# Kernel optimization log

Measured on AMD Instinct MI355X. Metric: run time of the kernel, lower is better.

## Reference

```python
import jax, jax.numpy as jnp
import numpy as np

N, M = 100000, 800000
F_IN, F_E, H = 64, 16, 64
T_NODE, T_EDGE = 2, 3
HEAD_DIM = 16.0


def setup_inputs() -> dict:
    key = jax.random.key(0)
    ks = jax.random.split(key, 16)
    inp = {
        "x": jax.random.normal(ks[0], (N, F_IN), jnp.float32),
        "edge_feat": jax.random.normal(ks[1], (M, F_E), jnp.float32),
        "node_type": jax.random.randint(ks[2], (N,), 0, T_NODE, jnp.int32),
        "edge_src": jax.random.randint(ks[3], (M,), 0, N, jnp.int32),
        "edge_dst": jax.random.randint(ks[4], (M,), 0, N, jnp.int32),
        "edge_type": jax.random.randint(ks[5], (M,), 0, T_EDGE, jnp.int32),
    }
    s_n = 1.0 / np.sqrt(F_IN)
    s_e = 1.0 / np.sqrt(F_E)
    for i, name in enumerate(["W1", "W2", "W3", "W4"]):
        inp[name] = jax.random.normal(ks[6 + i], (T_NODE, F_IN, H), jnp.float32) * s_n
        inp["b" + name[1]] = jax.random.normal(ks[10 + i], (T_NODE, H), jnp.float32) * 0.01
    inp["W5"] = jax.random.normal(ks[14], (T_EDGE, F_E, H), jnp.float32) * s_e
    inp["b5"] = jax.random.normal(ks[15], (T_EDGE, H), jnp.float32) * 0.01
    return inp


def _node_proj(x, W, b, node_type):
    # per-node-type linear: [T,F,H] weights, select row per node type
    p = jnp.einsum('nf,tfh->tnh', x, W) + b[:, None, :]      # [T,N,H]
    return jnp.take_along_axis(p, node_type[None, :, None], axis=0)[0]  # [N,H]


def reference(x, edge_feat, W1, b1, W2, b2, W3, b3, W4, b4, W5, b5,
              node_type, edge_src, edge_dst, edge_type):
    n = x.shape[0]
    h1 = _node_proj(x, W1, b1, node_type)
    h2 = _node_proj(x, W2, b2, node_type)
    h3 = _node_proj(x, W3, b3, node_type)
    h4 = _node_proj(x, W4, b4, node_type)
    # per-edge-type linear via weight gather (F_E is small)
    w5e = jnp.einsum('mf,mfh->mh', edge_feat, W5[edge_type]) + b5[edge_type]  # [M,H]
    # scalar attention logit per edge (w3_i . (w4_j + w5_ij)) / sqrt(head_dim)
    num = jnp.sum(h3[edge_dst] * (h4[edge_src] + w5e), axis=-1)  # [M]
    # softmax over a single scalar per edge == 1.0 exactly (faithful to source)
    score = jax.nn.softmax((num / jnp.sqrt(HEAD_DIM))[:, None], axis=-1)[:, 0]  # [M]
    msg = score[:, None] * (h2[edge_src] + w5e)                  # [M,H]
    out = h1 + jax.ops.segment_sum(msg, edge_dst, num_segments=n)
    return out
```

## Files before the change

### kernel.cpp

```cpp
#include <hip/hip_runtime.h>


#define CAP 16
#define OVF_CAP 32768

typedef __attribute__((ext_vector_type(8))) short short8;
typedef __attribute__((ext_vector_type(4))) float f32x4;

__device__ __forceinline__ float b2f(unsigned short u) {
    union { unsigned v; float f; } x; x.v = ((unsigned)u) << 16; return x.f;
}
__device__ __forceinline__ unsigned short f2b(float f) {
    union { float f; unsigned v; } x; x.f = f;
    unsigned u = x.v;
    unsigned r = (u + 0x7FFFu + ((u >> 16) & 1u)) >> 16;
    return (unsigned short)r;
}

__global__ __launch_bounds__(256) void k1_gemm_scatter(
    const float* __restrict__ x, const int* __restrict__ nt,
    const float* __restrict__ W1, const float* __restrict__ b1,
    const float* __restrict__ W2, const float* __restrict__ b2,
    const int* __restrict__ esrc, const int* __restrict__ edst,
    const int* __restrict__ etype,
    int* __restrict__ cnt32, int* __restrict__ ovfCnt,
    int4* __restrict__ ovf, int2* __restrict__ rec,
    float* __restrict__ out, unsigned short* __restrict__ h2b,
    int N, int M)
{
    __shared__ __align__(16) unsigned short sx[128 * 72];
    __shared__ __align__(16) unsigned short sw[4][64 * 72];
    __shared__ int snt[128];

    int tid = threadIdx.x;

    if (blockIdx.x & 1) {
        int e0 = (blockIdx.x >> 1) * 1024 + tid;
        int dd[4], ssrc[4], tty[4];
        bool v[4];
#pragma unroll
        for (int j = 0; j < 4; ++j) {
            int e = e0 + j * 256;
            v[j] = e < M;
            int ec = v[j] ? e : 0;
            dd[j]   = edst[ec];
            ssrc[j] = esrc[ec];
            tty[j]  = etype[ec];
        }
        int pos[4];
#pragma unroll
        for (int j = 0; j < 4; ++j)
            if (v[j]) pos[j] = atomicAdd(&cnt32[dd[j]], 1);
#pragma unroll
        for (int j = 0; j < 4; ++j) {
            if (!v[j]) continue;
            int packed = ssrc[j] | (tty[j] << 20);
            int e = e0 + j * 256;
            if (pos[j] < CAP) {
                rec[dd[j] * CAP + pos[j]] = make_int2(packed, e);
            } else {
                int slot = atomicAdd(ovfCnt, 1);
                if (slot < OVF_CAP) ovf[slot] = make_int4(packed, e, dd[j], 0);
            }
        }
        return;
    }

    int rowbase = (blockIdx.x >> 1) * 128;

    const float* Wm0 = W1;
    const float* Wm1 = W1 + 4096;
    const float* Wm2 = W2;
    const float* Wm3 = W2 + 4096;
#pragma unroll
    for (int j = 0; j < 4; ++j) {
        int k  = (tid >> 4) + j * 16;
        int n4 = (tid & 15) * 4;
        float4 w0 = *(const float4*)&Wm0[k * 64 + n4];
        float4 w1v = *(const float4*)&Wm1[k * 64 + n4];
        float4 w2v = *(const float4*)&Wm2[k * 64 + n4];
        float4 w3 = *(const float4*)&Wm3[k * 64 + n4];
        sw[0][(n4 + 0) * 72 + k] = f2b(w0.x);
        sw[0][(n4 + 1) * 72 + k] = f2b(w0.y);
        sw[0][(n4 + 2) * 72 + k] = f2b(w0.z);
        sw[0][(n4 + 3) * 72 + k] = f2b(w0.w);
        sw[1][(n4 + 0) * 72 + k] = f2b(w1v.x);
        sw[1][(n4 + 1) * 72 + k] = f2b(w1v.y);
        sw[1][(n4 + 2) * 72 + k] = f2b(w1v.z);
        sw[1][(n4 + 3) * 72 + k] = f2b(w1v.w);
        sw[2][(n4 + 0) * 72 + k] = f2b(w2v.x);
        sw[2][(n4 + 1) * 72 + k] = f2b(w2v.y);
        sw[2][(n4 + 2) * 72 + k] = f2b(w2v.z);
        sw[2][(n4 + 3) * 72 + k] = f2b(w2v.w);
        sw[3][(n4 + 0) * 72 + k] = f2b(w3.x);
        sw[3][(n4 + 1) * 72 + k] = f2b(w3.y);
        sw[3][(n4 + 2) * 72 + k] = f2b(w3.z);
        sw[3][(n4 + 3) * 72 + k] = f2b(w3.w);
    }

    if (tid < 128) {
        int r = rowbase + tid;
        snt[tid] = (r < N) ? nt[r] : 0;
    }

    int fr = (tid & 15) * 4;
    int ir = tid >> 4;
#pragma unroll
    for (int it = 0; it < 8; ++it) {
        int i = it * 16 + ir;
        int r = rowbase + i;
        float4 v = make_float4(0.f, 0.f, 0.f, 0.f);
        if (r < N) v = *(const float4*)&x[(size_t)r * 64 + fr];
        ushort4 p;
        p.x = f2b(v.x); p.y = f2b(v.y); p.z = f2b(v.z); p.w = f2b(v.w);
        *(ushort4*)&sx[i * 72 + fr] = p;
    }
    __syncthreads();

    int lane = tid & 63;
    int wid  = tid >> 6;
    int q    = lane >> 4;
    int cc   = lane & 15;
    int m0   = wid * 32;

    f32x4 acc[4][2][4];
#pragma unroll
    for (int mm = 0; mm < 4; ++mm)
#pragma unroll
        for (int s = 0; s < 2; ++s)
#pragma unroll
            for (int t = 0; t < 4; ++t)
                acc[mm][s][t] = (f32x4){0.f, 0.f, 0.f, 0.f};

#pragma unroll
    for (int k0 = 0; k0 < 64; k0 += 32) {
        int ko = k0 + q * 8;
        short8 af0 = *(short8*)&sx[(m0 + cc) * 72 + ko];
        short8 af1 = *(short8*)&sx[(m0 + 16 + cc) * 72 + ko];
#pragma unroll
        for (int mm = 0; mm < 4; ++mm)
#pragma unroll
            for (int t = 0; t < 4; ++t) {
                short8 bf = *(short8*)&sw[mm][(t * 16 + cc) * 72 + ko];
                acc[mm][0][t] = __builtin_amdgcn_mfma_f32_16x16x32_bf16(
                    af0, bf, acc[mm][0][t], 0, 0, 0);
                acc[mm][1][t] = __builtin_amdgcn_mfma_f32_16x16x32_bf16(
                    af1, bf, acc[mm][1][t], 0, 0, 0);
            }
    }

    float b1v[2][4], b2v[2][4];
#pragma unroll
    for (int ty = 0; ty < 2; ++ty)
#pragma unroll
        for (int t = 0; t < 4; ++t) {
            b1v[ty][t] = b1[ty * 64 + t * 16 + cc];
            b2v[ty][t] = b2[ty * 64 + t * 16 + cc];
        }

#pragma unroll
    for (int s = 0; s < 2; ++s)
#pragma unroll
        for (int reg = 0; reg < 4; ++reg) {
            int rl_ = m0 + s * 16 + q * 4 + reg;
            int r = rowbase + rl_;
            if (r < N) {
                int ty = snt[rl_];
#pragma unroll
                for (int t = 0; t < 4; ++t) {
                    float v1 = (ty ? acc[1][s][t][reg] : acc[0][s][t][reg])
                               + b1v[ty][t];
                    float v2 = (ty ? acc[3][s][t][reg] : acc[2][s][t][reg])
                               + b2v[ty][t];
                    out[(size_t)r * 64 + t * 16 + cc] = v1;
                    h2b[(size_t)r * 64 + t * 16 + cc] = f2b(v2);
                }
            }
        }
}

__global__ __launch_bounds__(256) void k2_gather(
    const float* __restrict__ ef, const int2* __restrict__ rec,
    const int* __restrict__ cnt32,
    const float* __restrict__ W5, const float* __restrict__ b5,
    const int4* __restrict__ ovf, const int* __restrict__ ovfCnt,
    const unsigned short* __restrict__ h2b, float* __restrict__ out,
    float* __restrict__ sacc,
    int N, int gatherBlocks, int ovfBlocks)
{
    int tid = threadIdx.x;
    int lane = tid & 63;
    int wid = tid >> 6;

    if (blockIdx.x >= (unsigned)gatherBlocks) {
        int novf = min(*ovfCnt, OVF_CAP);
        int gw = (blockIdx.x - gatherBlocks) * 4 + wid;
        int nw = ovfBlocks * 4;
        for (int ri = gw; ri < novf; ri += nw) {
            int4 o = ovf[ri];
            int s = o.x & 0xFFFFF;
            int t = (unsigned)o.x >> 20;
            float acc = b5[t * 64 + lane] + b2f(h2b[((size_t)s << 6) | lane]);
#pragma unroll
            for (int f = 0; f < 16; ++f)
                acc = fmaf(ef[(size_t)o.y * 16 + f],
                           W5[(t * 16 + f) * 64 + lane], acc);
            unsafeAtomicAdd(&out[(size_t)o.z * 64 + lane], acc);
        }
        return;
    }

    int d = blockIdx.x * 4 + wid;
    if (d >= N) return;

    int dg = min(cnt32[d], CAP);
    unsigned base = (unsigned)d * CAP;

    int myt = (lane < 48) ? (lane >> 4) : (lane - 48);
    unsigned myf = lane & 15;
    bool fl = lane < 48;
    float accH = 0.f, accS = 0.f;
    float hLast = 0.f, vLast = 0.f;
    int tLast = -1;
    int dgm1 = dg - 1;

    for (int i = 0; i < dg; i += 8) {
        int2 r[8];
#pragma unroll
        for (int j = 0; j < 8; ++j) {
            int ij = min(i + j, dgm1);
            r[j] = rec[base + ij];
        }
        float hv[8], ev[8];
#pragma unroll
        for (int j = 0; j < 8; ++j) {
            unsigned s = (unsigned)r[j].x & 0xFFFFFu;
            hv[j] = b2f(h2b[((size_t)s << 6) | (unsigned)lane]);
            ev[j] = ef[((unsigned)r[j].y << 4) | myf];
        }
#pragma unroll
        for (int j = 0; j < 8; ++j) {
            int t = (int)((unsigned)r[j].x >> 20);
            float v = fl ? ev[j] : 1.0f;
            accH += hv[j];
            accS += (t == myt) ? v : 0.f;
            hLast = hv[j]; vLast = v; tLast = t;
        }
    }
    float fd = (float)(((dg + 7) & ~7) - dg);
    accH -= fd * hLast;
    accS -= (tLast == myt) ? fd * vLast : 0.f;

    if (lane < 52)
        sacc[(size_t)d * 52 + lane] = accS;
    if (dg > 0)
        unsafeAtomicAdd(&out[((size_t)(unsigned)d << 6) | lane], accH);
}

__global__ __launch_bounds__(256) void k3_sacc_gemm(
    const float* __restrict__ sacc, const float* __restrict__ W5,
    const float* __restrict__ b5, float* __restrict__ out, int N)
{
    __shared__ __align__(16) unsigned short sa[128 * 136];
    __shared__ __align__(16) unsigned short swt[64 * 136];

    int tid = threadIdx.x;
    int rowbase = blockIdx.x * 128;

#pragma unroll
    for (int k = 0; k < 7; ++k) {
        int idx = tid + k * 256;
        if (idx < 1664) {
            int row = idx / 13;
            int q4 = (idx - row * 13) * 4;
            int d = rowbase + row;
            float4 v = make_float4(0.f, 0.f, 0.f, 0.f);
            if (d < N) v = *(const float4*)&sacc[(size_t)d * 52 + q4];
            ushort4 hi, lo;
            hi.x = f2b(v.x); lo.x = f2b(v.x - b2f(hi.x));
            hi.y = f2b(v.y); lo.y = f2b(v.y - b2f(hi.y));
            hi.z = f2b(v.z); lo.z = f2b(v.z - b2f(hi.z));
            hi.w = f2b(v.w); lo.w = f2b(v.w - b2f(hi.w));
            *(ushort4*)&sa[row * 136 + q4] = hi;
            *(ushort4*)&sa[row * 136 + 52 + q4] = lo;
        }
    }
    {
        ushort4 z; z.x = 0; z.y = 0; z.z = 0; z.w = 0;
#pragma unroll
        for (int k = 0; k < 3; ++k) {
            int idx = tid + k * 256;
            int row = idx / 6;
            int sp = (idx - row * 6) * 4;
            *(ushort4*)&sa[row * 136 + 104 + sp] = z;
        }
#pragma unroll
        for (int k = 0; k < 2; ++k) {
            int idx = tid + k * 256;
            if (idx < 384) {
                int h = idx / 6;
                int sp = (idx - h * 6) * 4;
                *(ushort4*)&swt[h * 136 + 104 + sp] = z;
            }
        }
    }
#pragma unroll
    for (int k = 0; k < 13; ++k) {
        int idx = tid + k * 256;
        int j = idx >> 6;
        int h = idx & 63;
        float wv = 0.f;
        if (j < 48)      wv = W5[j * 64 + h];
        else if (j < 51) wv = b5[(j - 48) * 64 + h];
        unsigned short wb = f2b(wv);
        swt[h * 136 + j] = wb;
        swt[h * 136 + 52 + j] = wb;
    }
    __syncthreads();

    int lane = tid & 63;
    int wid  = tid >> 6;
    int q    = lane >> 4;
    int cc   = lane & 15;
    int m0   = wid * 32;

    f32x4 acc[2][4];
#pragma unroll
    for (int s = 0; s < 2; ++s)
#pragma unroll
        for (int t = 0; t < 4; ++t)
            acc[s][t] = (f32x4){0.f, 0.f, 0.f, 0.f};

#pragma unroll
    for (int k0 = 0; k0 < 128; k0 += 32) {
        int ko = k0 + q * 8;
        short8 af0 = *(short8*)&sa[(m0 + cc) * 136 + ko];
        short8 af1 = *(short8*)&sa[(m0 + 16 + cc) * 136 + ko];
#pragma unroll
        for (int t = 0; t < 4; ++t) {
            short8 bf = *(short8*)&swt[(t * 16 + cc) * 136 + ko];
            acc[0][t] = __builtin_amdgcn_mfma_f32_16x16x32_bf16(
                af0, bf, acc[0][t], 0, 0, 0);
            acc[1][t] = __builtin_amdgcn_mfma_f32_16x16x32_bf16(
                af1, bf, acc[1][t], 0, 0, 0);
        }
    }

#pragma unroll
    for (int s = 0; s < 2; ++s)
#pragma unroll
        for (int reg = 0; reg < 4; ++reg) {
            int rl_ = m0 + s * 16 + q * 4 + reg;
            int r = rowbase + rl_;
            if (r < N) {
#pragma unroll
                for (int t = 0; t < 4; ++t) {
                    float* po = &out[(size_t)r * 64 + t * 16 + cc];
                    *po += acc[s][t][reg];
                }
            }
        }
}

extern "C" void kernel_launch(void* const* d_in, const int* in_sizes, int n_in,
                              void* d_out, int out_size, void* d_ws, size_t ws_size,
                              hipStream_t stream) {
    const float* x  = (const float*)d_in[0];
    const float* ef = (const float*)d_in[1];
    const int* nt   = (const int*)d_in[2];
    const int* es   = (const int*)d_in[3];
    const int* ed   = (const int*)d_in[4];
    const int* et   = (const int*)d_in[5];
    const float* W1 = (const float*)d_in[6];
    const float* b1 = (const float*)d_in[7];
    const float* W2 = (const float*)d_in[8];
    const float* b2 = (const float*)d_in[9];
    const float* W5 = (const float*)d_in[14];
    const float* b5 = (const float*)d_in[15];

    int N = in_sizes[2];
    int M = in_sizes[3];

    char* w = (char*)d_ws;
    size_t off = 0;
    unsigned short* h2b = (unsigned short*)(w + off); off += (size_t)N * 64 * 2;
    off = (off + 255) & ~(size_t)255;
    int2* rec = (int2*)(w + off); off += (size_t)N * CAP * 8;
    off = (off + 255) & ~(size_t)255;
    int4* ovf = (int4*)(w + off); off += (size_t)OVF_CAP * 16;
    off = (off + 255) & ~(size_t)255;
    float* sacc = (float*)(w + off); off += (size_t)N * 52 * 4;
    off = (off + 255) & ~(size_t)255;
    int* ovfCnt = (int*)(w + off);
    int* cnt32  = (int*)(w + off + 64);
    size_t zeroBytes = 64 + (size_t)N * 4;

    float* out = (float*)d_out;

    hipMemsetAsync(ovfCnt, 0, zeroBytes, stream);

    int gemmBlocks    = (N + 127) / 128;
    int scatterBlocks = (M + 1023) / 1024;
    int gb1 = 2 * max(gemmBlocks, scatterBlocks);
    k1_gemm_scatter<<<gb1, 256, 0, stream>>>(
        x, nt, W1, b1, W2, b2, es, ed, et,
        cnt32, ovfCnt, ovf, rec, out, h2b, N, M);

    int gatherBlocks = (N + 3) / 4;
    int ovfBlocks = 32;
    k2_gather<<<gatherBlocks + ovfBlocks, 256, 0, stream>>>(
        ef, rec, cnt32, W5, b5, ovf, ovfCnt, h2b, out, sacc,
        N, gatherBlocks, ovfBlocks);

    int k3Blocks = (N + 127) / 128;
    k3_sacc_gemm<<<k3Blocks, 256, 0, stream>>>(sacc, W5, b5, out, N);
}
```

Before: 314.3 us.

## Fuse per-node edge-feature GEMM into gather kernel, drop sacc round-trip

Merges the third kernel into the gather kernel. Each block now gathers 32 destination nodes, writes the per-type edge-feature sums as split hi/lo bf16 into shared memory, and runs the small MFMA GEMM against W5/b5 in the same block. It then atomically adds the GEMM result plus the h2 sum into the output. This removes the global sacc buffer write/read and one kernel launch. In exchange, each block rebuilds the W5 tile in LDS for only 32 rows (previously 128), uses more LDS per block, and processes 8 nodes serially per wave.

```diff
diff --git a/kernel.cpp b/kernel.cpp
--- a/kernel.cpp
+++ b/kernel.cpp
@@ -179,15 +179,18 @@
         }
 }
 
-__global__ __launch_bounds__(256) void k2_gather(
+__global__ __launch_bounds__(256) void k2_gather_mm(
     const float* __restrict__ ef, const int2* __restrict__ rec,
     const int* __restrict__ cnt32,
     const float* __restrict__ W5, const float* __restrict__ b5,
     const int4* __restrict__ ovf, const int* __restrict__ ovfCnt,
     const unsigned short* __restrict__ h2b, float* __restrict__ out,
-    float* __restrict__ sacc,
     int N, int gatherBlocks, int ovfBlocks)
 {
+    __shared__ __align__(16) unsigned short sa[32 * 136];
+    __shared__ __align__(16) unsigned short swt[64 * 136];
+    __shared__ __align__(16) float sH[32 * 66];
+
     int tid = threadIdx.x;
     int lane = tid & 63;
     int wid = tid >> 6;
@@ -210,100 +213,6 @@
         return;
     }
 
-    int d = blockIdx.x * 4 + wid;
-    if (d >= N) return;
-
-    int dg = min(cnt32[d], CAP);
-    unsigned base = (unsigned)d * CAP;
-
-    int myt = (lane < 48) ? (lane >> 4) : (lane - 48);
-    unsigned myf = lane & 15;
-    bool fl = lane < 48;
-    float accH = 0.f, accS = 0.f;
-    float hLast = 0.f, vLast = 0.f;
-    int tLast = -1;
-    int dgm1 = dg - 1;
-
-    for (int i = 0; i < dg; i += 8) {
-        int2 r[8];
-#pragma unroll
-        for (int j = 0; j < 8; ++j) {
-            int ij = min(i + j, dgm1);
-            r[j] = rec[base + ij];
-        }
-        float hv[8], ev[8];
-#pragma unroll
-        for (int j = 0; j < 8; ++j) {
-            unsigned s = (unsigned)r[j].x & 0xFFFFFu;
-            hv[j] = b2f(h2b[((size_t)s << 6) | (unsigned)lane]);
-            ev[j] = ef[((unsigned)r[j].y << 4) | myf];
-        }
-#pragma unroll
-        for (int j = 0; j < 8; ++j) {
-            int t = (int)((unsigned)r[j].x >> 20);
-            float v = fl ? ev[j] : 1.0f;
-            accH += hv[j];
-            accS += (t == myt) ? v : 0.f;
-            hLast = hv[j]; vLast = v; tLast = t;
-        }
-    }
-    float fd = (float)(((dg + 7) & ~7) - dg);
-    accH -= fd * hLast;
-    accS -= (tLast == myt) ? fd * vLast : 0.f;
-
-    if (lane < 52)
-        sacc[(size_t)d * 52 + lane] = accS;
-    if (dg > 0)
-        unsafeAtomicAdd(&out[((size_t)(unsigned)d << 6) | lane], accH);
-}
-
-__global__ __launch_bounds__(256) void k3_sacc_gemm(
-    const float* __restrict__ sacc, const float* __restrict__ W5,
-    const float* __restrict__ b5, float* __restrict__ out, int N)
-{
-    __shared__ __align__(16) unsigned short sa[128 * 136];
-    __shared__ __align__(16) unsigned short swt[64 * 136];
-
-    int tid = threadIdx.x;
-    int rowbase = blockIdx.x * 128;
-
-#pragma unroll
-    for (int k = 0; k < 7; ++k) {
-        int idx = tid + k * 256;
-        if (idx < 1664) {
-            int row = idx / 13;
-            int q4 = (idx - row * 13) * 4;
-            int d = rowbase + row;
-            float4 v = make_float4(0.f, 0.f, 0.f, 0.f);
-            if (d < N) v = *(const float4*)&sacc[(size_t)d * 52 + q4];
-            ushort4 hi, lo;
-            hi.x = f2b(v.x); lo.x = f2b(v.x - b2f(hi.x));
-            hi.y = f2b(v.y); lo.y = f2b(v.y - b2f(hi.y));
-            hi.z = f2b(v.z); lo.z = f2b(v.z - b2f(hi.z));
-            hi.w = f2b(v.w); lo.w = f2b(v.w - b2f(hi.w));
-            *(ushort4*)&sa[row * 136 + q4] = hi;
-            *(ushort4*)&sa[row * 136 + 52 + q4] = lo;
-        }
-    }
-    {
-        ushort4 z; z.x = 0; z.y = 0; z.z = 0; z.w = 0;
-#pragma unroll
-        for (int k = 0; k < 3; ++k) {
-            int idx = tid + k * 256;
-            int row = idx / 6;
-            int sp = (idx - row * 6) * 4;
-            *(ushort4*)&sa[row * 136 + 104 + sp] = z;
-        }
-#pragma unroll
-        for (int k = 0; k < 2; ++k) {
-            int idx = tid + k * 256;
-            if (idx < 384) {
-                int h = idx / 6;
-                int sp = (idx - h * 6) * 4;
-                *(ushort4*)&swt[h * 136 + 104 + sp] = z;
-            }
-        }
-    }
 #pragma unroll
     for (int k = 0; k < 13; ++k) {
         int idx = tid + k * 256;
@@ -316,50 +225,108 @@
         swt[h * 136 + j] = wb;
         swt[h * 136 + 52 + j] = wb;
     }
+    {
+        ushort4 z; z.x = 0; z.y = 0; z.z = 0; z.w = 0;
+#pragma unroll
+        for (int k = 0; k < 2; ++k) {
+            int idx = tid + k * 256;
+            if (idx < 384) {
+                int h = idx / 6;
+                int sp = (idx - h * 6) * 4;
+                *(ushort4*)&swt[h * 136 + 104 + sp] = z;
+            }
+        }
+        if (tid < 192) {
+            int row = tid / 6;
+            int sp = (tid - row * 6) * 4;
+            *(ushort4*)&sa[row * 136 + 104 + sp] = z;
+        }
+    }
+
+    int myt = (lane < 48) ? (lane >> 4) : (lane - 48);
+    unsigned myf = lane & 15;
+    bool fl = lane < 48;
+    int wbase = blockIdx.x * 32 + wid * 8;
+
+#pragma unroll 1
+    for (int g = 0; g < 8; ++g) {
+        int d = wbase + g;
+        int dg = (d < N) ? min(cnt32[d], CAP) : 0;
+        unsigned base = (unsigned)d * CAP;
+
+        float accH = 0.f, accS = 0.f;
+        float hLast = 0.f, vLast = 0.f;
+        int tLast = -1;
+        int dgm1 = dg - 1;
+
+        for (int i = 0; i < dg; i += 8) {
+            int2 r[8];
+#pragma unroll
+            for (int j = 0; j < 8; ++j) {
+                int ij = min(i + j, dgm1);
+                r[j] = rec[base + ij];
+            }
+            float hv[8], ev[8];
+#pragma unroll
+            for (int j = 0; j < 8; ++j) {
+                unsigned s = (unsigned)r[j].x & 0xFFFFFu;
+                hv[j] = b2f(h2b[((size_t)s << 6) | (unsigned)lane]);
+                ev[j] = ef[((unsigned)r[j].y << 4) | myf];
+            }
+#pragma unroll
+            for (int j = 0; j < 8; ++j) {
+                int t = (int)((unsigned)r[j].x >> 20);
+                float v = fl ? ev[j] : 1.0f;
+                accH += hv[j];
+                accS += (t == myt) ? v : 0.f;
+                hLast = hv[j]; vLast = v; tLast = t;
+            }
+        }
+        float fd = (float)(((dg + 7) & ~7) - dg);
+        accH -= fd * hLast;
+        accS -= (tLast == myt) ? fd * vLast : 0.f;
+
+        int wd = wid * 8 + g;
+        if (lane < 52) {
+            unsigned short hi = f2b(accS);
+            unsigned short lo = f2b(accS - b2f(hi));
+            sa[wd * 136 + lane] = hi;
+            sa[wd * 136 + 52 + lane] = lo;
+        }
+        sH[wd * 66 + lane] = accH;
+    }
     __syncthreads();
 
-    int lane = tid & 63;
-    int wid  = tid >> 6;
-    int q    = lane >> 4;
-    int cc   = lane & 15;
-    int m0   = wid * 32;
-
-    f32x4 acc[2][4];
-#pragma unroll
-    for (int s = 0; s < 2; ++s)
-#pragma unroll
-        for (int t = 0; t < 4; ++t)
-            acc[s][t] = (f32x4){0.f, 0.f, 0.f, 0.f};
-
+    int q  = lane >> 4;
+    int cc = lane & 15;
+    int s  = wid & 1;
+    int t0 = wid >> 1;
+
+    f32x4 acc0 = (f32x4){0.f, 0.f, 0.f, 0.f};
+    f32x4 acc1 = (f32x4){0.f, 0.f, 0.f, 0.f};
 #pragma unroll
     for (int k0 = 0; k0 < 128; k0 += 32) {
         int ko = k0 + q * 8;
-        short8 af0 = *(short8*)&sa[(m0 + cc) * 136 + ko];
-        short8 af1 = *(short8*)&sa[(m0 + 16 + cc) * 136 + ko];
-#pragma unroll
-        for (int t = 0; t < 4; ++t) {
-            short8 bf = *(short8*)&swt[(t * 16 + cc) * 136 + ko];
-            acc[0][t] = __builtin_amdgcn_mfma_f32_16x16x32_bf16(
-                af0, bf, acc[0][t], 0, 0, 0);
-            acc[1][t] = __builtin_amdgcn_mfma_f32_16x16x32_bf16(
-                af1, bf, acc[1][t], 0, 0, 0);
-        }
-    }
-
-#pragma unroll
-    for (int s = 0; s < 2; ++s)
-#pragma unroll
-        for (int reg = 0; reg < 4; ++reg) {
-            int rl_ = m0 + s * 16 + q * 4 + reg;
-            int r = rowbase + rl_;
-            if (r < N) {
-#pragma unroll
-                for (int t = 0; t < 4; ++t) {
-                    float* po = &out[(size_t)r * 64 + t * 16 + cc];
-                    *po += acc[s][t][reg];
-                }
-            }
-        }
+        short8 af = *(short8*)&sa[(s * 16 + cc) * 136 + ko];
+        short8 bf0 = *(short8*)&swt[(t0 * 16 + cc) * 136 + ko];
+        short8 bf1 = *(short8*)&swt[((t0 + 2) * 16 + cc) * 136 + ko];
+        acc0 = __builtin_amdgcn_mfma_f32_16x16x32_bf16(af, bf0, acc0, 0, 0, 0);
+        acc1 = __builtin_amdgcn_mfma_f32_16x16x32_bf16(af, bf1, acc1, 0, 0, 0);
+    }
+
+#pragma unroll
+    for (int reg = 0; reg < 4; ++reg) {
+        int rl = s * 16 + q * 4 + reg;
+        int d = blockIdx.x * 32 + rl;
+        if (d < N) {
+            int c0 = t0 * 16 + cc;
+            int c1 = (t0 + 2) * 16 + cc;
+            float v0 = acc0[reg] + sH[rl * 66 + c0];
+            float v1 = acc1[reg] + sH[rl * 66 + c1];
+            unsafeAtomicAdd(&out[(size_t)d * 64 + c0], v0);
+            unsafeAtomicAdd(&out[(size_t)d * 64 + c1], v1);
+        }
+    }
 }
 
 extern "C" void kernel_launch(void* const* d_in, const int* in_sizes, int n_in,
@@ -389,8 +356,6 @@
     off = (off + 255) & ~(size_t)255;
     int4* ovf = (int4*)(w + off); off += (size_t)OVF_CAP * 16;
     off = (off + 255) & ~(size_t)255;
-    float* sacc = (float*)(w + off); off += (size_t)N * 52 * 4;
-    off = (off + 255) & ~(size_t)255;
     int* ovfCnt = (int*)(w + off);
     int* cnt32  = (int*)(w + off + 64);
     size_t zeroBytes = 64 + (size_t)N * 4;
@@ -406,12 +371,9 @@
         x, nt, W1, b1, W2, b2, es, ed, et,
         cnt32, ovfCnt, ovf, rec, out, h2b, N, M);
 
-    int gatherBlocks = (N + 3) / 4;
+    int gatherBlocks = (N + 31) / 32;
     int ovfBlocks = 32;
-    k2_gather<<<gatherBlocks + ovfBlocks, 256, 0, stream>>>(
-        ef, rec, cnt32, W5, b5, ovf, ovfCnt, h2b, out, sacc,
+    k2_gather_mm<<<gatherBlocks + ovfBlocks, 256, 0, stream>>>(
+        ef, rec, cnt32, W5, b5, ovf, ovfCnt, h2b, out,
         N, gatherBlocks, ovfBlocks);
-
-    int k3Blocks = (N + 127) / 128;
-    k3_sacc_gemm<<<k3Blocks, 256, 0, stream>>>(sacc, W5, b5, out, N);
-}
+}
```

Measured after the change: 309.3 us. No clear change (-1.6%).
